# Kernel tuning notes

Measured on AMD Instinct MI355X. Metric: run time of the kernel, lower is better.

## Reference

```python
import jax, jax.numpy as jnp
import numpy as np
import math

IN_F, OUT_F = 4096, 4096
ORDER, TENSOR_RANK = 4, 8
LEAF_A = math.ceil(IN_F ** (1.0 / ORDER))   # 8
LEAF_B = math.ceil(OUT_F ** (1.0 / ORDER))  # 8


def setup_inputs() -> dict:
    key = jax.random.key(0)
    k1, k2, k3, k4 = jax.random.split(key, 4)
    x = jax.random.normal(k1, (8, 2048, IN_F), dtype=jnp.float32)
    weight = jax.random.normal(k2, (OUT_F, IN_F), dtype=jnp.float32) * 0.02
    bias = jax.random.normal(k3, (OUT_F,), dtype=jnp.float32) * 0.02
    # reset_parameters: gain for leaky_relu(sqrt(5)) = sqrt(2/(1+5)); std = gain / in_features**(1/order)
    gain = math.sqrt(2.0 / (1.0 + 5.0))
    std = gain / (IN_F ** (1.0 / ORDER))
    weight_leafs = jax.random.uniform(
        k4, (ORDER, TENSOR_RANK, LEAF_A, LEAF_B), dtype=jnp.float32,
        minval=-std, maxval=std)
    return {"x": x, "weight": weight, "bias": bias, "weight_leafs": weight_leafs}


def _reproduce_weight(weight_leafs):
    # Original einsum 'lij,rmn->rimjn' sums the FIRST operand over its leading
    # (rank) axis; chained through both stages + final .sum(0), every leaf is
    # summed over tensor_rank. Exact math = nested Kronecker of the rank-summed
    # leaves, sliced to [:in_features, :out_features].
    s = weight_leafs.sum(axis=1)  # (4, a, b)
    a, b = LEAF_A, LEAF_B
    z1 = jnp.einsum('ij,mn->imjn', s[0], s[1]).reshape(a * a, b * b)
    z2 = jnp.einsum('ij,mn->imjn', s[2], s[3]).reshape(a * a, b * b)
    zzz = jnp.einsum('ij,mn->imjn', z1, z2).reshape(a ** 4, b ** 4)
    return zzz[:IN_F, :OUT_F]  # (in_features, out_features)


def reference(x, weight, bias, weight_leafs):
    tensor_weight = _reproduce_weight(weight_leafs)       # (in, out)
    full_weight = weight + tensor_weight.T                # (out, in)
    # F.linear: x @ W^T + b
    return jnp.einsum('bsi,oi->bso', x, full_weight) + bias
```

## Files before the change

kernel.cpp:

```cpp
#include <hip/hip_runtime.h>
#include <hip/hip_bf16.h>
#include <stdint.h>

typedef __attribute__((ext_vector_type(8))) __bf16 bf16x8;
typedef __attribute__((ext_vector_type(4))) float f32x4;

#define IN_F   4096
#define OUT_F  4096
#define M_ROWS 16384

static __device__ __forceinline__ unsigned short f2bf(float f) {
    unsigned int u = __float_as_uint(f);
    u += 0x7FFFu + ((u >> 16) & 1u);
    return (unsigned short)(u >> 16);
}

__global__ __launch_bounds__(256) void build_w_kernel(
    const float* __restrict__ weight, const float* __restrict__ leafs,
    unsigned short* __restrict__ wb)
{
    __shared__ float s[4][8][8];
    const int t = threadIdx.x;
    {
        const int o = t >> 6, a = (t >> 3) & 7, b = t & 7;
        float acc = 0.f;
        #pragma unroll
        for (int r = 0; r < 8; ++r)
            acc += leafs[o * 512 + r * 64 + a * 8 + b];
        s[o][a][b] = acc;
    }
    __syncthreads();

    const int total = (OUT_F * IN_F) / 8;
    for (int idx = blockIdx.x * 256 + t; idx < total; idx += gridDim.x * 256) {
        const int n  = idx >> 9;
        const int kg = idx & 511;
        const int n0 = n >> 9, n1 = (n >> 6) & 7, n2 = (n >> 3) & 7, n3 = n & 7;
        const int k0 = kg >> 6, k1 = (kg >> 3) & 7, k2 = kg & 7;
        const float p = s[0][k0][n0] * s[1][k1][n1] * s[2][k2][n2];
        const float4* wp = (const float4*)(weight + (size_t)n * IN_F + kg * 8);
        const float4 w0 = wp[0], w1 = wp[1];
        const float wv[8] = {w0.x, w0.y, w0.z, w0.w, w1.x, w1.y, w1.z, w1.w};
        unsigned int pk[4];
        #pragma unroll
        for (int j = 0; j < 4; ++j) {
            unsigned int lo = f2bf(wv[2*j]   + p * s[3][2*j]  [n3]);
            unsigned int hi = f2bf(wv[2*j+1] + p * s[3][2*j+1][n3]);
            pk[j] = lo | (hi << 16);
        }
        *reinterpret_cast<uint4*>(wb + (size_t)n * IN_F + kg * 8) =
            make_uint4(pk[0], pk[1], pk[2], pk[3]);
    }
}

__global__ __launch_bounds__(256) void conv_x_kernel(
    const float* __restrict__ x, unsigned short* __restrict__ xb, long long n8)
{
    for (long long idx = (long long)blockIdx.x * 256 + threadIdx.x; idx < n8;
         idx += (long long)gridDim.x * 256) {
        const float4* xp = (const float4*)(x + idx * 8);
        const float4 a = xp[0], b = xp[1];
        const float v[8] = {a.x, a.y, a.z, a.w, b.x, b.y, b.z, b.w};
        unsigned int pk[4];
        #pragma unroll
        for (int j = 0; j < 4; ++j)
            pk[j] = (unsigned int)f2bf(v[2*j]) | ((unsigned int)f2bf(v[2*j+1]) << 16);
        *reinterpret_cast<uint4*>(xb + idx * 8) = make_uint4(pk[0], pk[1], pk[2], pk[3]);
    }
}

#define BK 64
#define NT (IN_F / BK)

#define PANEL_A(b,kk) (ldsb + ((b)*2+(kk))*16384)
#define PANEL_B(b,kk) (ldsb + 65536 + ((b)*2+(kk))*16384)

#define GLL(src, dst) __builtin_amdgcn_global_load_lds( \
    (const __attribute__((address_space(1))) void*)(src), \
    (__attribute__((address_space(3))) void*)(dst), 16, 0, 0)

#define STAGE_A(b, kk, ko) do { \
    GLL(sA1 + (ko) + (kk)*32, PANEL_A(b,kk) + d1); \
    GLL(sA2 + (ko) + (kk)*32, PANEL_A(b,kk) + d2); } while(0)
#define STAGE_B(b, kk, ko) do { \
    GLL(sB1 + (ko) + (kk)*32, PANEL_B(b,kk) + d1); \
    GLL(sB2 + (ko) + (kk)*32, PANEL_B(b,kk) + d2); } while(0)

__global__ __launch_bounds__(512, 2) void gemm8_kernel(
    const unsigned short* __restrict__ xb,
    const unsigned short* __restrict__ wb,
    const float* __restrict__ bias,
    float* __restrict__ out)
{
    __shared__ unsigned short lds_us[65536];
    char* const ldsb = (char*)lds_us;

    const int t    = threadIdx.x;
    const int wave = t >> 6;
    const int lane = t & 63;
    const int lr   = lane & 15;
    const int kq   = lane >> 4;
    const int wr   = wave >> 2;
    const int wcn  = wave & 3;
    const int sx   = (lr & 6) << 3;

    const int nwg  = gridDim.x;
    const int bid  = blockIdx.x;
    const int swzb = (bid & 7) * (nwg >> 3) + (bid >> 3);
    const int bm   = (swzb & 63) * 256;
    const int bn   = (swzb >> 6) * 256;

    const int c1 = t, c2 = t + 512;
    const int r1 = c1 >> 2, r2 = c2 >> 2;
    const int q1 = ((c1 & 3) * 16) ^ ((r1 & 6) << 3);
    const int q2 = ((c2 & 3) * 16) ^ ((r2 & 6) << 3);
    const unsigned short* sA1 = xb + (size_t)(bm + r1) * IN_F + (q1 >> 1);
    const unsigned short* sA2 = xb + (size_t)(bm + r2) * IN_F + (q2 >> 1);
    const unsigned short* sB1 = wb + (size_t)(bn + r1) * IN_F + (q1 >> 1);
    const unsigned short* sB2 = wb + (size_t)(bn + r2) * IN_F + (q2 >> 1);
    const int d1 = c1 * 16, d2 = c2 * 16;

    const int aro = (wr * 128 + lr) * 64 + ((kq * 16) ^ sx);
    const int bro = (wcn * 64 + lr) * 64 + ((kq * 16) ^ sx);

    f32x4 acc[8][4] = {};

    STAGE_A(0, 0, 0); STAGE_B(0, 0, 0); STAGE_A(0, 1, 0); STAGE_B(0, 1, 0);
    asm volatile("s_waitcnt vmcnt(4)" ::: "memory");
    __builtin_amdgcn_s_barrier();

    for (int tt = 0; tt < NT; ++tt) {
        const int cur = tt & 1;
        const int nxt = cur ^ 1;
        const int ko  = (tt + 1) * BK;
        const bool pf = (tt + 1 < NT);
        const char* pA0 = PANEL_A(cur, 0);
        const char* pA1 = PANEL_A(cur, 1);
        const char* pB0 = PANEL_B(cur, 0);
        const char* pB1 = PANEL_B(cur, 1);

        bf16x8 af[4], bf[4];

        #pragma unroll
        for (int m = 0; m < 4; ++m)
            af[m] = *(const bf16x8*)(pA0 + aro + m * 1024);
        #pragma unroll
        for (int n = 0; n < 4; ++n)
            bf[n] = *(const bf16x8*)(pB0 + bro + n * 1024);
        if (pf) STAGE_A(nxt, 0, ko);
        __builtin_amdgcn_s_barrier();
        asm volatile("s_waitcnt lgkmcnt(0)" ::: "memory");
        __builtin_amdgcn_sched_barrier(0);
        __builtin_amdgcn_s_setprio(1);
        #pragma unroll
        for (int m = 0; m < 4; ++m)
            #pragma unroll
            for (int n = 0; n < 4; ++n)
                acc[m][n] = __builtin_amdgcn_mfma_f32_16x16x32_bf16(
                    af[m], bf[n], acc[m][n], 0, 0, 0);
        __builtin_amdgcn_s_setprio(0);
        __builtin_amdgcn_s_barrier();

        #pragma unroll
        for (int m = 0; m < 4; ++m)
            af[m] = *(const bf16x8*)(pA0 + aro + (m + 4) * 1024);
        if (pf) STAGE_B(nxt, 0, ko);
        __builtin_amdgcn_s_barrier();
        asm volatile("s_waitcnt lgkmcnt(0)" ::: "memory");
        __builtin_amdgcn_sched_barrier(0);
        __builtin_amdgcn_s_setprio(1);
        #pragma unroll
        for (int m = 0; m < 4; ++m)
            #pragma unroll
            for (int n = 0; n < 4; ++n)
                acc[m + 4][n] = __builtin_amdgcn_mfma_f32_16x16x32_bf16(
                    af[m], bf[n], acc[m + 4][n], 0, 0, 0);
        __builtin_amdgcn_s_setprio(0);
        if (pf) asm volatile("s_waitcnt vmcnt(4)" ::: "memory");
        else    asm volatile("s_waitcnt vmcnt(0)" ::: "memory");
        __builtin_amdgcn_s_barrier();

        #pragma unroll
        for (int m = 0; m < 4; ++m)
            af[m] = *(const bf16x8*)(pA1 + aro + m * 1024);
        #pragma unroll
        for (int n = 0; n < 4; ++n)
            bf[n] = *(const bf16x8*)(pB1 + bro + n * 1024);
        if (pf) STAGE_A(nxt, 1, ko);
        __builtin_amdgcn_s_barrier();
        asm volatile("s_waitcnt lgkmcnt(0)" ::: "memory");
        __builtin_amdgcn_sched_barrier(0);
        __builtin_amdgcn_s_setprio(1);
        #pragma unroll
        for (int m = 0; m < 4; ++m)
            #pragma unroll
            for (int n = 0; n < 4; ++n)
                acc[m][n] = __builtin_amdgcn_mfma_f32_16x16x32_bf16(
                    af[m], bf[n], acc[m][n], 0, 0, 0);
        __builtin_amdgcn_s_setprio(0);
        __builtin_amdgcn_s_barrier();

        #pragma unroll
        for (int m = 0; m < 4; ++m)
            af[m] = *(const bf16x8*)(pA1 + aro + (m + 4) * 1024);
        if (pf) STAGE_B(nxt, 1, ko);
        __builtin_amdgcn_s_barrier();
        asm volatile("s_waitcnt lgkmcnt(0)" ::: "memory");
        __builtin_amdgcn_sched_barrier(0);
        __builtin_amdgcn_s_setprio(1);
        #pragma unroll
        for (int m = 0; m < 4; ++m)
            #pragma unroll
            for (int n = 0; n < 4; ++n)
                acc[m + 4][n] = __builtin_amdgcn_mfma_f32_16x16x32_bf16(
                    af[m], bf[n], acc[m + 4][n], 0, 0, 0);
        __builtin_amdgcn_s_setprio(0);
        if (pf) asm volatile("s_waitcnt vmcnt(4)" ::: "memory");
        else    asm volatile("s_waitcnt vmcnt(0)" ::: "memory");
        __builtin_amdgcn_s_barrier();
    }

    #pragma unroll
    for (int n = 0; n < 4; ++n) {
        const int col = bn + wcn * 64 + n * 16 + lr;
        const float bv = bias[col];
        #pragma unroll
        for (int m = 0; m < 8; ++m) {
            const size_t rb = (size_t)(bm + wr * 128 + m * 16 + kq * 4) * OUT_F + col;
            #pragma unroll
            for (int j = 0; j < 4; ++j)
                out[rb + (size_t)j * OUT_F] = acc[m][n][j] + bv;
        }
    }
}

#define FBM 128
#define FBN 128
#define FBK 32

__global__ __launch_bounds__(256) void gemm_fb_kernel(
    const float* __restrict__ xf,
    const unsigned short* __restrict__ wb,
    const float* __restrict__ bias,
    float* __restrict__ out)
{
    __shared__ unsigned short As[FBM * FBK];
    __shared__ unsigned short Bs[FBN * FBK];

    const int t    = threadIdx.x;
    const int wave = t >> 6;
    const int lane = t & 63;
    const int lr   = lane & 15;
    const int kq   = lane >> 4;
    const int wr   = wave >> 1;
    const int wc   = wave & 1;

    const int bm = blockIdx.x * FBM;
    const int bn = blockIdx.y * FBN;
    const int srow = t >> 2;
    const int scol = (t & 3) * 8;

    f32x4 acc[4][4] = {};

    for (int kt = 0; kt < IN_F; kt += FBK) {
        #pragma unroll
        for (int g = 0; g < 2; ++g) {
            const int row = srow + g * 64;
            const float4* xp = (const float4*)(xf + (size_t)(bm + row) * IN_F + kt + scol);
            const float4 a0 = xp[0], a1 = xp[1];
            const float v[8] = {a0.x, a0.y, a0.z, a0.w, a1.x, a1.y, a1.z, a1.w};
            unsigned int pk[4];
            #pragma unroll
            for (int j = 0; j < 4; ++j)
                pk[j] = (unsigned int)f2bf(v[2*j]) | ((unsigned int)f2bf(v[2*j+1]) << 16);
            *reinterpret_cast<uint4*>(&As[row * FBK + scol]) =
                make_uint4(pk[0], pk[1], pk[2], pk[3]);
        }
        {
            const unsigned short* gb0 = wb + (size_t)(bn + srow) * IN_F + kt + scol;
            const unsigned short* gb1 = gb0 + (size_t)64 * IN_F;
            GLL(gb0, Bs + srow * FBK + scol);
            GLL(gb1, Bs + (64 + srow) * FBK + scol);
        }
        __syncthreads();

        bf16x8 af[4], bfr[4];
        #pragma unroll
        for (int m = 0; m < 4; ++m)
            af[m] = *reinterpret_cast<const bf16x8*>(As + (wr * 64 + m * 16 + lr) * FBK + kq * 8);
        #pragma unroll
        for (int n = 0; n < 4; ++n)
            bfr[n] = *reinterpret_cast<const bf16x8*>(Bs + (wc * 64 + n * 16 + lr) * FBK + kq * 8);

        #pragma unroll
        for (int m = 0; m < 4; ++m)
            #pragma unroll
            for (int n = 0; n < 4; ++n)
                acc[m][n] = __builtin_amdgcn_mfma_f32_16x16x32_bf16(af[m], bfr[n], acc[m][n], 0, 0, 0);

        __syncthreads();
    }

    const int crow0 = kq * 4;
    #pragma unroll
    for (int n = 0; n < 4; ++n) {
        const int col = bn + wc * 64 + n * 16 + lr;
        const float bv = bias[col];
        #pragma unroll
        for (int m = 0; m < 4; ++m) {
            const int rowb = bm + wr * 64 + m * 16 + crow0;
            #pragma unroll
            for (int j = 0; j < 4; ++j)
                out[(size_t)(rowb + j) * OUT_F + col] = acc[m][n][j] + bv;
        }
    }
}

extern "C" void kernel_launch(void* const* d_in, const int* in_sizes, int n_in,
                              void* d_out, int out_size, void* d_ws, size_t ws_size,
                              hipStream_t stream) {
    const float* x      = (const float*)d_in[0];
    const float* weight = (const float*)d_in[1];
    const float* bias   = (const float*)d_in[2];
    const float* leafs  = (const float*)d_in[3];
    float* out = (float*)d_out;

    unsigned short* wb = (unsigned short*)d_ws;
    unsigned short* xbuf = (unsigned short*)((char*)d_ws +
                           (size_t)OUT_F * IN_F * sizeof(unsigned short));

    const size_t need_full = (size_t)OUT_F * IN_F * 2 + (size_t)M_ROWS * IN_F * 2;
    const bool full = ws_size >= need_full;

    build_w_kernel<<<dim3(2048), dim3(256), 0, stream>>>(weight, leafs, wb);

    if (full) {
        conv_x_kernel<<<dim3(2048), dim3(256), 0, stream>>>(
            x, xbuf, (long long)M_ROWS * IN_F / 8);
        gemm8_kernel<<<dim3((M_ROWS / 256) * (OUT_F / 256)), dim3(512), 0, stream>>>(
            xbuf, wb, bias, out);
    } else {
        gemm_fb_kernel<<<dim3(M_ROWS / FBM, OUT_F / FBN), dim3(256), 0, stream>>>(
            x, wb, bias, out);
    }
}
```

Before: 650.8 us.

## Software-pipeline LDS fragment loads across MFMA phases with partial waitcnts

Restructures the GEMM main loop into a macro-unrolled TILE that double-buffers A fragments in registers (aP/aQ), so the next LDS reads are issued before the current MFMA block and waited on with partial lgkmcnt. Removes the extra barrier before each MFMA group, hardcodes the grid swizzle and tile counts as constants, and simplifies the staging address arithmetic to one base pointer plus a fixed offset. The goal is to hide LDS latency behind MFMA work and cut synchronisation. In exchange it raises register pressure and depends on the fine-grained waitcnt counts being exactly right.

Result: faster. 590.2 us (-9.3%).

```diff
diff --git a/kernel.cpp b/kernel.cpp
--- a/kernel.cpp
+++ b/kernel.cpp
@@ -70,7 +70,7 @@
 }
 
 #define BK 64
-#define NT (IN_F / BK)
+#define NT 64
 
 #define PANEL_A(b,kk) (ldsb + ((b)*2+(kk))*16384)
 #define PANEL_B(b,kk) (ldsb + 65536 + ((b)*2+(kk))*16384)
@@ -80,11 +80,63 @@
     (__attribute__((address_space(3))) void*)(dst), 16, 0, 0)
 
 #define STAGE_A(b, kk, ko) do { \
-    GLL(sA1 + (ko) + (kk)*32, PANEL_A(b,kk) + d1); \
-    GLL(sA2 + (ko) + (kk)*32, PANEL_A(b,kk) + d2); } while(0)
+    GLL(sA1 + (ko) + (kk)*32,          PANEL_A(b,kk) + d1); \
+    GLL(sA1 + 524288 + (ko) + (kk)*32, PANEL_A(b,kk) + d1 + 8192); } while(0)
 #define STAGE_B(b, kk, ko) do { \
-    GLL(sB1 + (ko) + (kk)*32, PANEL_B(b,kk) + d1); \
-    GLL(sB2 + (ko) + (kk)*32, PANEL_B(b,kk) + d2); } while(0)
+    GLL(sB1 + (ko) + (kk)*32,          PANEL_B(b,kk) + d1); \
+    GLL(sB1 + 524288 + (ko) + (kk)*32, PANEL_B(b,kk) + d1 + 8192); } while(0)
+
+#define SB0  __builtin_amdgcn_sched_barrier(0)
+#define BAR  __builtin_amdgcn_s_barrier()
+#define PRI1 __builtin_amdgcn_s_setprio(1)
+#define PRI0 __builtin_amdgcn_s_setprio(0)
+#define WLG4 asm volatile("s_waitcnt lgkmcnt(4)" ::: "memory")
+#define WLG0 asm volatile("s_waitcnt lgkmcnt(0)" ::: "memory")
+#define WVM2 asm volatile("s_waitcnt vmcnt(2)" ::: "memory")
+#define WVM0 asm volatile("s_waitcnt vmcnt(0)" ::: "memory")
+
+#define LDA(dst, BUF, KK, MH) do { _Pragma("unroll") \
+    for (int i_ = 0; i_ < 4; ++i_) \
+        dst[i_] = *(const bf16x8*)(aB + ((BUF)*32768 + (KK)*16384 + ((MH)*4+i_)*1024)); } while(0)
+#define LDB(dst, BUF, KK) do { _Pragma("unroll") \
+    for (int i_ = 0; i_ < 4; ++i_) \
+        dst[i_] = *(const bf16x8*)(bB + ((BUF)*32768 + (KK)*16384 + i_*1024)); } while(0)
+#define MM(AS, MH) do { _Pragma("unroll") \
+    for (int m_ = 0; m_ < 4; ++m_) { _Pragma("unroll") \
+    for (int n_ = 0; n_ < 4; ++n_) \
+        acc[(MH)*4+m_][n_] = __builtin_amdgcn_mfma_f32_16x16x32_bf16( \
+            AS[m_], bF[n_], acc[(MH)*4+m_][n_], 0, 0, 0); } } while(0)
+
+#define TILE(BUF, KO, PF) do { \
+     \
+    LDB(bF, BUF, 0); \
+    LDA(aQ, BUF, 0, 1); \
+    if (PF) STAGE_A((BUF)^1, 0, KO); \
+    SB0; WLG4; SB0; \
+    PRI1; MM(aP, 0); PRI0; SB0; \
+    if (PF) { WVM2; } else { WVM0; } \
+    BAR; SB0; \
+     \
+    LDA(aP, BUF, 1, 0); \
+    if (PF) STAGE_B((BUF)^1, 0, KO); \
+    SB0; WLG4; SB0; \
+    PRI1; MM(aQ, 1); PRI0; SB0; \
+    BAR; SB0; \
+     \
+    LDB(bF, BUF, 1); \
+    LDA(aQ, BUF, 1, 1); \
+    if (PF) STAGE_A((BUF)^1, 1, KO); \
+    SB0; WLG4; SB0; \
+    PRI1; MM(aP, 0); PRI0; SB0; \
+    if (PF) { WVM2; } else { WVM0; } \
+    BAR; SB0; \
+     \
+    if (PF) { LDA(aP, (BUF)^1, 0, 0); STAGE_B((BUF)^1, 1, KO); SB0; WLG4; } \
+    else    { SB0; WLG0; } \
+    SB0; \
+    PRI1; MM(aQ, 1); PRI0; SB0; \
+    BAR; SB0; \
+} while (0)
 
 __global__ __launch_bounds__(512, 2) void gemm8_kernel(
     const unsigned short* __restrict__ xb,
@@ -104,121 +156,38 @@
     const int wcn  = wave & 3;
     const int sx   = (lr & 6) << 3;
 
-    const int nwg  = gridDim.x;
     const int bid  = blockIdx.x;
-    const int swzb = (bid & 7) * (nwg >> 3) + (bid >> 3);
-    const int bm   = (swzb & 63) * 256;
-    const int bn   = (swzb >> 6) * 256;
-
-    const int c1 = t, c2 = t + 512;
-    const int r1 = c1 >> 2, r2 = c2 >> 2;
+    const int swzb = (bid & 7) * 128 + (bid >> 3);
+    const int bm   = (swzb >> 4) * 256;
+    const int bn   = (swzb & 15) * 256;
+
+    const int c1 = t;
+    const int r1 = c1 >> 2;
     const int q1 = ((c1 & 3) * 16) ^ ((r1 & 6) << 3);
-    const int q2 = ((c2 & 3) * 16) ^ ((r2 & 6) << 3);
     const unsigned short* sA1 = xb + (size_t)(bm + r1) * IN_F + (q1 >> 1);
-    const unsigned short* sA2 = xb + (size_t)(bm + r2) * IN_F + (q2 >> 1);
     const unsigned short* sB1 = wb + (size_t)(bn + r1) * IN_F + (q1 >> 1);
-    const unsigned short* sB2 = wb + (size_t)(bn + r2) * IN_F + (q2 >> 1);
-    const int d1 = c1 * 16, d2 = c2 * 16;
-
-    const int aro = (wr * 128 + lr) * 64 + ((kq * 16) ^ sx);
-    const int bro = (wcn * 64 + lr) * 64 + ((kq * 16) ^ sx);
+    const int d1 = c1 * 16;
+
+    const char* aB = ldsb + (wr * 128 + lr) * 64 + ((kq * 16) ^ sx);
+    const char* bB = ldsb + 65536 + (wcn * 64 + lr) * 64 + ((kq * 16) ^ sx);
 
     f32x4 acc[8][4] = {};
+    bf16x8 aP[4], aQ[4], bF[4];
 
     STAGE_A(0, 0, 0); STAGE_B(0, 0, 0); STAGE_A(0, 1, 0); STAGE_B(0, 1, 0);
     asm volatile("s_waitcnt vmcnt(4)" ::: "memory");
-    __builtin_amdgcn_s_barrier();
-
-    for (int tt = 0; tt < NT; ++tt) {
-        const int cur = tt & 1;
-        const int nxt = cur ^ 1;
-        const int ko  = (tt + 1) * BK;
-        const bool pf = (tt + 1 < NT);
-        const char* pA0 = PANEL_A(cur, 0);
-        const char* pA1 = PANEL_A(cur, 1);
-        const char* pB0 = PANEL_B(cur, 0);
-        const char* pB1 = PANEL_B(cur, 1);
-
-        bf16x8 af[4], bf[4];
-
-        #pragma unroll
-        for (int m = 0; m < 4; ++m)
-            af[m] = *(const bf16x8*)(pA0 + aro + m * 1024);
-        #pragma unroll
-        for (int n = 0; n < 4; ++n)
-            bf[n] = *(const bf16x8*)(pB0 + bro + n * 1024);
-        if (pf) STAGE_A(nxt, 0, ko);
-        __builtin_amdgcn_s_barrier();
-        asm volatile("s_waitcnt lgkmcnt(0)" ::: "memory");
-        __builtin_amdgcn_sched_barrier(0);
-        __builtin_amdgcn_s_setprio(1);
-        #pragma unroll
-        for (int m = 0; m < 4; ++m)
-            #pragma unroll
-            for (int n = 0; n < 4; ++n)
-                acc[m][n] = __builtin_amdgcn_mfma_f32_16x16x32_bf16(
-                    af[m], bf[n], acc[m][n], 0, 0, 0);
-        __builtin_amdgcn_s_setprio(0);
-        __builtin_amdgcn_s_barrier();
-
-        #pragma unroll
-        for (int m = 0; m < 4; ++m)
-            af[m] = *(const bf16x8*)(pA0 + aro + (m + 4) * 1024);
-        if (pf) STAGE_B(nxt, 0, ko);
-        __builtin_amdgcn_s_barrier();
-        asm volatile("s_waitcnt lgkmcnt(0)" ::: "memory");
-        __builtin_amdgcn_sched_barrier(0);
-        __builtin_amdgcn_s_setprio(1);
-        #pragma unroll
-        for (int m = 0; m < 4; ++m)
-            #pragma unroll
-            for (int n = 0; n < 4; ++n)
-                acc[m + 4][n] = __builtin_amdgcn_mfma_f32_16x16x32_bf16(
-                    af[m], bf[n], acc[m + 4][n], 0, 0, 0);
-        __builtin_amdgcn_s_setprio(0);
-        if (pf) asm volatile("s_waitcnt vmcnt(4)" ::: "memory");
-        else    asm volatile("s_waitcnt vmcnt(0)" ::: "memory");
-        __builtin_amdgcn_s_barrier();
-
-        #pragma unroll
-        for (int m = 0; m < 4; ++m)
-            af[m] = *(const bf16x8*)(pA1 + aro + m * 1024);
-        #pragma unroll
-        for (int n = 0; n < 4; ++n)
-            bf[n] = *(const bf16x8*)(pB1 + bro + n * 1024);
-        if (pf) STAGE_A(nxt, 1, ko);
-        __builtin_amdgcn_s_barrier();
-        asm volatile("s_waitcnt lgkmcnt(0)" ::: "memory");
-        __builtin_amdgcn_sched_barrier(0);
-        __builtin_amdgcn_s_setprio(1);
-        #pragma unroll
-        for (int m = 0; m < 4; ++m)
-            #pragma unroll
-            for (int n = 0; n < 4; ++n)
-                acc[m][n] = __builtin_amdgcn_mfma_f32_16x16x32_bf16(
-                    af[m], bf[n], acc[m][n], 0, 0, 0);
-        __builtin_amdgcn_s_setprio(0);
-        __builtin_amdgcn_s_barrier();
-
-        #pragma unroll
-        for (int m = 0; m < 4; ++m)
-            af[m] = *(const bf16x8*)(pA1 + aro + (m + 4) * 1024);
-        if (pf) STAGE_B(nxt, 1, ko);
-        __builtin_amdgcn_s_barrier();
-        asm volatile("s_waitcnt lgkmcnt(0)" ::: "memory");
-        __builtin_amdgcn_sched_barrier(0);
-        __builtin_amdgcn_s_setprio(1);
-        #pragma unroll
-        for (int m = 0; m < 4; ++m)
-            #pragma unroll
-            for (int n = 0; n < 4; ++n)
-                acc[m + 4][n] = __builtin_amdgcn_mfma_f32_16x16x32_bf16(
-                    af[m], bf[n], acc[m + 4][n], 0, 0, 0);
-        __builtin_amdgcn_s_setprio(0);
-        if (pf) asm volatile("s_waitcnt vmcnt(4)" ::: "memory");
-        else    asm volatile("s_waitcnt vmcnt(0)" ::: "memory");
-        __builtin_amdgcn_s_barrier();
-    }
+    BAR; SB0;
+    LDA(aP, 0, 0, 0);
+
+    #pragma unroll 1
+    for (int tt = 0; tt < NT - 2; tt += 2) {
+        const int ko0 = (tt + 1) * BK;
+        const int ko1 = (tt + 2) * BK;
+        TILE(0, ko0, true);
+        TILE(1, ko1, true);
+    }
+    TILE(0, (NT - 1) * BK, true);
+    TILE(1, 0, false);
 
     #pragma unroll
     for (int n = 0; n < 4; ++n) {
```
